# Kernel tuning notes

Hardware: AMD Instinct MI355X
Metric: run time of the kernel (lower is better)

The kernel has to match this reference:

```python
import jax, jax.numpy as jnp
import numpy as np

NEG_INF = -jnp.inf


def _mlp(x, W1, b1, W2, b2, W3, b3):
    h = jax.nn.relu(x @ W1 + b1)
    h = jax.nn.relu(h @ W2 + b2)
    return h @ W3 + b3


def setup_inputs() -> dict:
    key = jax.random.key(0)
    ks = jax.random.split(key, 8)
    B, D, H, A = 65536, 1024, 128, 47
    obs_tensor = jax.random.normal(ks[0], (B, D), jnp.float32)
    action_mask = jax.random.randint(ks[1], (B, 2, A), 0, 2).astype(jnp.int32)
    action_mask = action_mask.at[:, :, 0].set(1)  # pass action always legal
    def lin(k, fan_in, shape):
        s = 1.0 / np.sqrt(fan_in)
        return jax.random.uniform(k, shape, jnp.float32, -s, s)
    W1 = lin(ks[2], D, (D, H)); b1 = lin(ks[3], D, (H,))
    W2 = lin(ks[4], H, (H, H)); b2 = lin(ks[5], H, (H,))
    W3 = lin(ks[6], H, (H, 2 * A)); b3 = lin(ks[7], H, (2 * A,))
    return {"obs_tensor": obs_tensor, "action_mask": action_mask,
            "W1": W1, "b1": b1, "W2": W2, "b2": b2, "W3": W3, "b3": b3}


def reference(obs_tensor, action_mask, W1, b1, W2, b2, W3, b3):
    B = obs_tensor.shape[0]
    A = W3.shape[1] // 2
    logits = _mlp(obs_tensor.reshape(B, -1), W1, b1, W2, b2, W3, b3).reshape(B, 2, A)
    logits = jnp.where(action_mask == 0, NEG_INF, logits)

    fp1 = (action_mask[:, 0].sum(axis=1) == 1) & (action_mask[:, 0, 0] == 1)
    fp2 = (action_mask[:, 1].sum(axis=1) == 1) & (action_mask[:, 1, 0] == 1)

    idx = jnp.arange(A)
    k1, k2 = jax.random.split(jax.random.key(42))
    g1 = jax.random.gumbel(k1, (B, A), jnp.float32)
    g2 = jax.random.gumbel(k2, (B, A), jnp.float32)

    # side 1: when force_pass_2 (and not force_pass_1), index 0 is removed before sampling
    l1 = logits[:, 0]
    l1 = jnp.where((fp2 & ~fp1)[:, None] & (idx[None, :] == 0), NEG_INF, l1)
    a1_sampled = jnp.argmax(l1 + g1, axis=1)
    a1 = jnp.where(fp1, 0, a1_sampled)

    # side 2 extra masking driven by sampled action1 (default branch only)
    switch1 = (a1 >= 1) & (a1 <= 6)
    move1 = (a1 >= 27) & (a1 <= 46)
    extra = (switch1[:, None] & (idx[None, :] == a1[:, None])) | \
            (move1[:, None] & (idx[None, :] >= 27) & (idx[None, :] < 46))
    mask2 = ((fp1 & ~fp2)[:, None] & (idx[None, :] == 0)) | \
            ((~fp1 & ~fp2)[:, None] & extra)
    l2 = jnp.where(mask2, NEG_INF, logits[:, 1])
    a2_sampled = jnp.argmax(l2 + g2, axis=1)
    a2 = jnp.where(fp2, 0, a2_sampled)

    return jnp.stack([a1, a2], axis=1).astype(jnp.int64)
```

## Files before the change

kernel.cpp:

```cpp
#include <hip/hip_runtime.h>

typedef unsigned int u32;
typedef unsigned long long u64;
typedef _Float16 f16;
typedef f16 half8 __attribute__((ext_vector_type(8)));
typedef float f32x4 __attribute__((ext_vector_type(4)));

struct U2 { u32 x, y; };

__host__ __device__ constexpr u32 rotl32(u32 v, int r) {
  return (v << r) | (v >> (32 - r));
}

__host__ __device__ constexpr U2 threefry2x32(u32 k0, u32 k1, u32 c0, u32 c1) {
  u32 ks2 = k0 ^ k1 ^ 0x1BD11BDAu;
  u32 x0 = c0 + k0, x1 = c1 + k1;
#define TFR(r) { x0 += x1; x1 = rotl32(x1, r); x1 ^= x0; }
  TFR(13) TFR(15) TFR(26) TFR(6)
  x0 += k1; x1 += ks2 + 1u;
  TFR(17) TFR(29) TFR(16) TFR(24)
  x0 += ks2; x1 += k0 + 2u;
  TFR(13) TFR(15) TFR(26) TFR(6)
  x0 += k0; x1 += k1 + 3u;
  TFR(17) TFR(29) TFR(16) TFR(24)
  x0 += k1; x1 += ks2 + 4u;
  TFR(13) TFR(15) TFR(26) TFR(6)
  x0 += ks2; x1 += k0 + 5u;
#undef TFR
  return {x0, x1};
}

constexpr U2 SK1 = threefry2x32(0u, 42u, 0u, 0u);
constexpr U2 SK2 = threefry2x32(0u, 42u, 0u, 1u);
constexpr u32 K1A = SK1.x, K1B = SK1.y;
constexpr u32 K2A = SK2.x, K2B = SK2.y;

#define NACT 47

__device__ __forceinline__ float gumbel_at(u32 kA, u32 kB, u32 i) {
  U2 r = threefry2x32(kA, kB, 0u, i);
  u32 bits = r.x ^ r.y;
  float f = __uint_as_float(0x3f800000u | (bits >> 9)) - 1.0f;
  f = fmaxf(f, 1.17549435e-38f);
  return -logf(-logf(f));
}

__device__ __forceinline__ u32 fmono(float f) {
  u32 b = __float_as_uint(f);
  return b ^ ((b & 0x80000000u) ? 0xFFFFFFFFu : 0x80000000u);
}

#define W1H_OFF 0u
#define W1L_OFF 262144u
#define W2H_OFF 524288u
#define W2L_OFF 557056u
#define W3H_OFF 589824u
#define W3L_OFF 614400u
#define WS_NEEDED 638976u

__global__ __launch_bounds__(256)
void prep_weights(const float* __restrict__ W1, const float* __restrict__ W2,
                  const float* __restrict__ W3, char* __restrict__ ws) {
  const int bid = blockIdx.x, t = threadIdx.x;
  if (bid < 512) {
    int idx = bid * 256 + t;
    int col = idx & 127, k = idx >> 7;
    float w = W1[(size_t)k * 128 + col] * 32.0f;
    f16 h = (f16)w;
    f16 l = (f16)((w - (float)h) * 2048.0f);
    u32 addr = (u32)(k >> 6) * 16384u + (u32)(col >> 4) * 2048u +
               (u32)((k >> 5) & 1) * 1024u + (u32)((k >> 3) & 3) * 256u +
               (u32)(col & 15) * 16u + (u32)(k & 7) * 2u;
    *(f16*)(ws + W1H_OFF + addr) = h;
    *(f16*)(ws + W1L_OFF + addr) = l;
  } else if (bid < 576) {
    int idx = (bid - 512) * 256 + t;
    int col = idx & 127, k = idx >> 7;
    float w = W2[(size_t)k * 128 + col] * 32.0f;
    f16 h = (f16)w;
    f16 l = (f16)((w - (float)h) * 2048.0f);
    u32 addr = (u32)(k >> 5) * 8192u + (u32)(col >> 4) * 1024u +
               (u32)((k >> 3) & 3) * 256u + (u32)(col & 15) * 16u + (u32)(k & 7) * 2u;
    *(f16*)(ws + W2H_OFF + addr) = h;
    *(f16*)(ws + W2L_OFF + addr) = l;
  } else {
    int idx = (bid - 576) * 256 + t;
    int col = idx % 96, k = idx / 96;
    float w = (col < 94) ? W3[(size_t)k * 94 + col] * 32.0f : 0.0f;
    f16 h = (f16)w;
    f16 l = (f16)((w - (float)h) * 2048.0f);
    u32 addr = (u32)(k >> 5) * 6144u + (u32)(col >> 4) * 1024u +
               (u32)((k >> 3) & 3) * 256u + (u32)(col & 15) * 16u + (u32)(k & 7) * 2u;
    *(f16*)(ws + W3H_OFF + addr) = h;
    *(f16*)(ws + W3L_OFF + addr) = l;
  }
}

__device__ __forceinline__ f32x4 mfma16(half8 a, half8 b, f32x4 c) {
  return __builtin_amdgcn_mfma_f32_16x16x32_f16(a, b, c, 0, 0, 0);
}

__device__ __forceinline__ void split8(float4 v0, float4 v1, half8& hi, half8& lo) {
  float xs[8] = {v0.x, v0.y, v0.z, v0.w, v1.x, v1.y, v1.z, v1.w};
#pragma unroll
  for (int i = 0; i < 8; i++) {
    f16 h = (f16)xs[i];
    hi[i] = h;
    lo[i] = (f16)((xs[i] - (float)h) * 2048.0f);
  }
}

__device__ __forceinline__ u32 hb_addr(int row, int g8) {
  return (u32)row * 128u + (u32)((g8 ^ (row & 15)) << 3);
}

__global__ __launch_bounds__(256, 4)
void fused_mfma(const float* __restrict__ X, const int* __restrict__ AM,
                const float* __restrict__ b1, const float* __restrict__ b2,
                const float* __restrict__ b3, const char* __restrict__ ws,
                int* __restrict__ out) {
  __shared__ __align__(16) char smem[32768];
  const int t = threadIdx.x;
  const int lane = t & 63, wid = t >> 6;
  const int lrow = lane & 15, g = lane >> 4;
  const int wr = wid & 1, wc = wid >> 1;
  const int rowBase = blockIdx.x * 64;
  float* Hb = (float*)smem;

  f32x4 mainA[2][4], crossA[2][4];
#pragma unroll
  for (int ti = 0; ti < 2; ti++)
#pragma unroll
    for (int tc = 0; tc < 4; tc++)
#pragma unroll
      for (int r = 0; r < 4; r++) { mainA[ti][tc][r] = 0.0f; crossA[ti][tc][r] = 0.0f; }

  {
    const int rowS = t >> 2, gq = t & 3;
    const float* xsrc = X + (size_t)(rowBase + rowS) * 1024 + gq * 8;
    const u32 wadr = (u32)rowS * 72u + (u32)gq * 16u;
    const u32 radr0 = (u32)(32 * wr + lrow) * 72u + (u32)g * 16u;
    const u32 radr1 = (u32)(32 * wr + 16 + lrow) * 72u + (u32)g * 16u;
    const char* wbase = ws + W1H_OFF + (u32)(4 * wc) * 2048u + (u32)g * 256u + (u32)lrow * 16u;

    float4 sx0, sx1;
    sx0 = *(const float4*)(xsrc);
    sx1 = *(const float4*)(xsrc + 4);
    {
      half8 h, l;
      split8(sx0, sx1, h, l);
      *(half8*)(smem + wadr) = h;
      *(half8*)(smem + wadr + 4608) = l;
    }
    sx0 = *(const float4*)(xsrc + 32);
    sx1 = *(const float4*)(xsrc + 36);
    __syncthreads();

    for (int ks = 0; ks < 32; ks++) {
      const u32 cur = (u32)(ks & 1) * 9216u;
      if (ks < 31) {
        const u32 nxt = (u32)((ks + 1) & 1) * 9216u;
        half8 h, l;
        split8(sx0, sx1, h, l);
        *(half8*)(smem + nxt + wadr) = h;
        *(half8*)(smem + nxt + wadr + 4608) = l;
        if (ks < 30) {
          sx0 = *(const float4*)(xsrc + (ks + 2) * 32);
          sx1 = *(const float4*)(xsrc + (ks + 2) * 32 + 4);
        }
      }
      half8 ah0 = *(const half8*)(smem + cur + radr0);
      half8 al0 = *(const half8*)(smem + cur + radr0 + 4608);
      half8 ah1 = *(const half8*)(smem + cur + radr1);
      half8 al1 = *(const half8*)(smem + cur + radr1 + 4608);
      const char* wb = wbase + (u32)(ks >> 1) * 16384u + (u32)(ks & 1) * 1024u;
#pragma unroll
      for (int tc = 0; tc < 4; tc++) {
        half8 bh = *(const half8*)(wb + tc * 2048);
        half8 bl = *(const half8*)(wb + 262144 + tc * 2048);
        mainA[0][tc]  = mfma16(ah0, bh, mainA[0][tc]);
        crossA[0][tc] = mfma16(ah0, bl, crossA[0][tc]);
        crossA[0][tc] = mfma16(al0, bh, crossA[0][tc]);
        mainA[1][tc]  = mfma16(ah1, bh, mainA[1][tc]);
        crossA[1][tc] = mfma16(ah1, bl, crossA[1][tc]);
        crossA[1][tc] = mfma16(al1, bh, crossA[1][tc]);
      }
      __syncthreads();
    }
  }
#pragma unroll
  for (int ti = 0; ti < 2; ti++)
#pragma unroll
    for (int tc = 0; tc < 4; tc++) {
      const int col = 64 * wc + 16 * tc + lrow;
      const int g8 = col >> 3, c7 = col & 7;
      const float bb = b1[col];
#pragma unroll
      for (int r = 0; r < 4; r++) {
        const int row = 32 * wr + 16 * ti + 4 * g + r;
        Hb[hb_addr(row, g8) + c7] =
            fmaxf((mainA[ti][tc][r] + crossA[ti][tc][r] * 4.8828125e-4f) * 0.03125f + bb,
                  0.0f);
        mainA[ti][tc][r] = 0.0f; crossA[ti][tc][r] = 0.0f;
      }
    }
  __syncthreads();

  {
    const char* wbase = ws + W2H_OFF + (u32)(4 * wc) * 1024u + (u32)g * 256u + (u32)lrow * 16u;
    for (int cc = 0; cc < 4; cc++) {
      half8 ah[2], al[2];
#pragma unroll
      for (int ti = 0; ti < 2; ti++) {
        const int row = 32 * wr + 16 * ti + lrow;
        const float* hp = Hb + hb_addr(row, 4 * cc + g);
        split8(*(const float4*)hp, *(const float4*)(hp + 4), ah[ti], al[ti]);
      }
      const char* wb = wbase + (u32)cc * 8192u;
#pragma unroll
      for (int tc = 0; tc < 4; tc++) {
        half8 bh = *(const half8*)(wb + tc * 1024);
        half8 bl = *(const half8*)(wb + 32768 + tc * 1024);
#pragma unroll
        for (int ti = 0; ti < 2; ti++) {
          mainA[ti][tc]  = mfma16(ah[ti], bh, mainA[ti][tc]);
          crossA[ti][tc] = mfma16(ah[ti], bl, crossA[ti][tc]);
          crossA[ti][tc] = mfma16(al[ti], bh, crossA[ti][tc]);
        }
      }
    }
  }
  __syncthreads();
#pragma unroll
  for (int ti = 0; ti < 2; ti++)
#pragma unroll
    for (int tc = 0; tc < 4; tc++) {
      const int col = 64 * wc + 16 * tc + lrow;
      const int g8 = col >> 3, c7 = col & 7;
      const float bb = b2[col];
#pragma unroll
      for (int r = 0; r < 4; r++) {
        const int row = 32 * wr + 16 * ti + 4 * g + r;
        Hb[hb_addr(row, g8) + c7] =
            fmaxf((mainA[ti][tc][r] + crossA[ti][tc][r] * 4.8828125e-4f) * 0.03125f + bb,
                  0.0f);
        mainA[ti][tc][r] = 0.0f; crossA[ti][tc][r] = 0.0f;
      }
    }
  __syncthreads();

  f32x4 main3[2][3], cross3[2][3];
#pragma unroll
  for (int ti = 0; ti < 2; ti++)
#pragma unroll
    for (int tc = 0; tc < 3; tc++)
#pragma unroll
      for (int r = 0; r < 4; r++) { main3[ti][tc][r] = 0.0f; cross3[ti][tc][r] = 0.0f; }
  {
    const char* wbase = ws + W3H_OFF + (u32)(3 * wc) * 1024u + (u32)g * 256u + (u32)lrow * 16u;
    for (int cc = 0; cc < 4; cc++) {
      half8 ah[2], al[2];
#pragma unroll
      for (int ti = 0; ti < 2; ti++) {
        const int row = 32 * wr + 16 * ti + lrow;
        const float* hp = Hb + hb_addr(row, 4 * cc + g);
        split8(*(const float4*)hp, *(const float4*)(hp + 4), ah[ti], al[ti]);
      }
      const char* wb = wbase + (u32)cc * 6144u;
#pragma unroll
      for (int tc = 0; tc < 3; tc++) {
        half8 bh = *(const half8*)(wb + tc * 1024);
        half8 bl = *(const half8*)(wb + 24576 + tc * 1024);
#pragma unroll
        for (int ti = 0; ti < 2; ti++) {
          main3[ti][tc]  = mfma16(ah[ti], bh, main3[ti][tc]);
          cross3[ti][tc] = mfma16(ah[ti], bl, cross3[ti][tc]);
          cross3[ti][tc] = mfma16(al[ti], bh, cross3[ti][tc]);
        }
      }
    }
  }
  __syncthreads();

  float* Ls = (float*)smem;
#pragma unroll
  for (int ti = 0; ti < 2; ti++)
#pragma unroll
    for (int tc = 0; tc < 3; tc++) {
      const int col = 48 * wc + 16 * tc + lrow;
      const float bb = (col < 94) ? b3[col] : 0.0f;
#pragma unroll
      for (int r = 0; r < 4; r++) {
        const int row = 32 * wr + 16 * ti + 4 * g + r;
        Ls[row * 97 + col] =
            (main3[ti][tc][r] + cross3[ti][tc][r] * 4.8828125e-4f) * 0.03125f + bb;
      }
    }
  __syncthreads();

  {
    const int row = 16 * wid + lrow;
    const int q = g;
    const int* amg = AM + (size_t)(rowBase + row) * 94;
    const float* ls = Ls + row * 97;
    const float NI = -__builtin_huge_valf();

    int amv1[12], amv2[12];
    int s0 = 0, s1 = 0;
#pragma unroll
    for (int k = 0; k < 12; k++) {
      const int a = q + 4 * k;
      amv1[k] = (a < NACT) ? amg[a] : 0;
      amv2[k] = (a < NACT) ? amg[NACT + a] : 0;
      s0 += amv1[k]; s1 += amv2[k];
    }
    s0 += __shfl_xor(s0, 16); s0 += __shfl_xor(s0, 32);
    s1 += __shfl_xor(s1, 16); s1 += __shfl_xor(s1, 32);
    const int am0 = amg[0], amN = amg[NACT];
    const bool fp1 = (s0 == 1) && (am0 == 1);
    const bool fp2 = (s1 == 1) && (amN == 1);
    const u32 growA = (u32)(rowBase + row) * 47u;

    u64 best = 0;
#pragma unroll
    for (int k = 0; k < 12; k++) {
      const int a = q + 4 * k;
      if (a >= NACT) break;
      float l = (amv1[k] != 0) ? ls[a] : NI;
      if (fp2 && !fp1 && a == 0) l = NI;
      float v = l + gumbel_at(K1A, K1B, growA + (u32)a);
      u64 key = ((u64)fmono(v) << 6) | (u32)(63 - a);
      if (key > best) best = key;
    }
    u64 o = __shfl_xor(best, 16); if (o > best) best = o;
    o = __shfl_xor(best, 32); if (o > best) best = o;
    const int a1 = fp1 ? 0 : (63 - (int)(best & 63u));

    const bool sw1 = (a1 >= 1) && (a1 <= 6);
    const bool mv1 = (a1 >= 27);
    best = 0;
#pragma unroll
    for (int k = 0; k < 12; k++) {
      const int a = q + 4 * k;
      if (a >= NACT) break;
      float l = (amv2[k] != 0) ? ls[NACT + a] : NI;
      bool extra = (sw1 && a == a1) || (mv1 && a >= 27 && a < 46);
      if ((fp1 && !fp2 && a == 0) || (!fp1 && !fp2 && extra)) l = NI;
      float v = l + gumbel_at(K2A, K2B, growA + (u32)a);
      u64 key = ((u64)fmono(v) << 6) | (u32)(63 - a);
      if (key > best) best = key;
    }
    o = __shfl_xor(best, 16); if (o > best) best = o;
    o = __shfl_xor(best, 32); if (o > best) best = o;
    const int a2 = fp2 ? 0 : (63 - (int)(best & 63u));

    if (q == 0) {
      out[(size_t)(rowBase + row) * 2 + 0] = a1;
      out[(size_t)(rowBase + row) * 2 + 1] = a2;
    }
  }
}

__global__ __launch_bounds__(256)
void fused_policy_v1(const float* __restrict__ X,  const int* __restrict__ AM,
                     const float* __restrict__ W1, const float* __restrict__ b1,
                     const float* __restrict__ W2, const float* __restrict__ b2,
                     const float* __restrict__ W3, const float* __restrict__ b3,
                     int* __restrict__ out) {
  __shared__ alignas(16) char smem[59904];
  float (*HT)[68]   = reinterpret_cast<float (*)[68]>(smem);
  float (*Wst)[128] = reinterpret_cast<float (*)[128]>(smem + 34816);
  float (*Ws3)[96]  = reinterpret_cast<float (*)[96]>(smem + 34816);
  float (*Xt)[68]   = reinterpret_cast<float (*)[68]>(smem + 51200);
  float (*Lsr)[97]  = reinterpret_cast<float (*)[97]>(smem);
  int*   Amf        = reinterpret_cast<int*>(smem + 34816);

  const int t = threadIdx.x;
  const int rowBase = blockIdx.x * 64;
  const int tx = t & 31, ty = t >> 5;
  const int c0 = tx * 4, r0 = ty * 8;

  float accf[8][4]; double accd[8][4];
#pragma unroll
  for (int i = 0; i < 8; i++)
#pragma unroll
    for (int j = 0; j < 4; j++) { accf[i][j] = 0.0f; accd[i][j] = 0.0; }

  for (int k0 = 0; k0 < 1024; k0 += 32) {
#pragma unroll
    for (int i = 0; i < 2; i++) {
      int idx = t + i * 256;
      int row = idx >> 3, kb = (idx & 7) * 4;
      float4 v = *reinterpret_cast<const float4*>(X + (size_t)(rowBase + row) * 1024 + k0 + kb);
      Xt[kb + 0][row] = v.x; Xt[kb + 1][row] = v.y;
      Xt[kb + 2][row] = v.z; Xt[kb + 3][row] = v.w;
    }
#pragma unroll
    for (int i = 0; i < 4; i++) {
      int idx = t + i * 256;
      int kr = idx >> 5, c4 = (idx & 31) * 4;
      *reinterpret_cast<float4*>(&Wst[kr][c4]) =
          *reinterpret_cast<const float4*>(W1 + (size_t)(k0 + kr) * 128 + c4);
    }
    __syncthreads();
#pragma unroll
    for (int kk = 0; kk < 32; kk++) {
      float4 a0 = *reinterpret_cast<const float4*>(&Xt[kk][r0]);
      float4 a1 = *reinterpret_cast<const float4*>(&Xt[kk][r0 + 4]);
      float4 b  = *reinterpret_cast<const float4*>(&Wst[kk][c0]);
      float av[8] = {a0.x, a0.y, a0.z, a0.w, a1.x, a1.y, a1.z, a1.w};
      float bv[4] = {b.x, b.y, b.z, b.w};
#pragma unroll
      for (int i = 0; i < 8; i++)
#pragma unroll
        for (int j = 0; j < 4; j++) accf[i][j] = fmaf(av[i], bv[j], accf[i][j]);
    }
    if ((k0 & 63) == 32) {
#pragma unroll
      for (int i = 0; i < 8; i++)
#pragma unroll
        for (int j = 0; j < 4; j++) { accd[i][j] += (double)accf[i][j]; accf[i][j] = 0.0f; }
    }
    __syncthreads();
  }
  {
    const float4 bv = *reinterpret_cast<const float4*>(b1 + c0);
#pragma unroll
    for (int i = 0; i < 8; i++) {
      HT[c0 + 0][r0 + i] = fmaxf((float)accd[i][0] + bv.x, 0.0f);
      HT[c0 + 1][r0 + i] = fmaxf((float)accd[i][1] + bv.y, 0.0f);
      HT[c0 + 2][r0 + i] = fmaxf((float)accd[i][2] + bv.z, 0.0f);
      HT[c0 + 3][r0 + i] = fmaxf((float)accd[i][3] + bv.w, 0.0f);
    }
  }
  __syncthreads();

#pragma unroll
  for (int i = 0; i < 8; i++)
#pragma unroll
    for (int j = 0; j < 4; j++) { accf[i][j] = 0.0f; accd[i][j] = 0.0; }
  for (int k0 = 0; k0 < 128; k0 += 32) {
#pragma unroll
    for (int i = 0; i < 4; i++) {
      int idx = t + i * 256;
      int kr = idx >> 5, c4 = (idx & 31) * 4;
      *reinterpret_cast<float4*>(&Wst[kr][c4]) =
          *reinterpret_cast<const float4*>(W2 + (size_t)(k0 + kr) * 128 + c4);
    }
    __syncthreads();
#pragma unroll
    for (int kk = 0; kk < 32; kk++) {
      float4 a0 = *reinterpret_cast<const float4*>(&HT[k0 + kk][r0]);
      float4 a1 = *reinterpret_cast<const float4*>(&HT[k0 + kk][r0 + 4]);
      float4 b  = *reinterpret_cast<const float4*>(&Wst[kk][c0]);
      float av[8] = {a0.x, a0.y, a0.z, a0.w, a1.x, a1.y, a1.z, a1.w};
      float bv[4] = {b.x, b.y, b.z, b.w};
#pragma unroll
      for (int i = 0; i < 8; i++)
#pragma unroll
        for (int j = 0; j < 4; j++) accf[i][j] = fmaf(av[i], bv[j], accf[i][j]);
    }
    if ((k0 & 63) == 32) {
#pragma unroll
      for (int i = 0; i < 8; i++)
#pragma unroll
        for (int j = 0; j < 4; j++) { accd[i][j] += (double)accf[i][j]; accf[i][j] = 0.0f; }
    }
    __syncthreads();
  }
  {
    const float4 bv = *reinterpret_cast<const float4*>(b2 + c0);
#pragma unroll
    for (int i = 0; i < 8; i++) {
      HT[c0 + 0][r0 + i] = fmaxf((float)accd[i][0] + bv.x, 0.0f);
      HT[c0 + 1][r0 + i] = fmaxf((float)accd[i][1] + bv.y, 0.0f);
      HT[c0 + 2][r0 + i] = fmaxf((float)accd[i][2] + bv.z, 0.0f);
      HT[c0 + 3][r0 + i] = fmaxf((float)accd[i][3] + bv.w, 0.0f);
    }
  }
  __syncthreads();

  const int c3 = tx * 3;
  float acc3f[8][3]; double acc3d[8][3];
#pragma unroll
  for (int i = 0; i < 8; i++)
#pragma unroll
    for (int j = 0; j < 3; j++) { acc3f[i][j] = 0.0f; acc3d[i][j] = 0.0; }
  for (int k0 = 0; k0 < 128; k0 += 32) {
#pragma unroll
    for (int i = 0; i < 12; i++) {
      int idx = t + i * 256;
      int kr = idx / 96, c = idx - kr * 96;
      Ws3[kr][c] = (c < 94) ? W3[(size_t)(k0 + kr) * 94 + c] : 0.0f;
    }
    __syncthreads();
#pragma unroll
    for (int kk = 0; kk < 32; kk++) {
      float4 a0 = *reinterpret_cast<const float4*>(&HT[k0 + kk][r0]);
      float4 a1 = *reinterpret_cast<const float4*>(&HT[k0 + kk][r0 + 4]);
      float b0 = Ws3[kk][c3], b1v = Ws3[kk][c3 + 1], b2v = Ws3[kk][c3 + 2];
      float av[8] = {a0.x, a0.y, a0.z, a0.w, a1.x, a1.y, a1.z, a1.w};
      float bv3[3] = {b0, b1v, b2v};
#pragma unroll
      for (int i = 0; i < 8; i++)
#pragma unroll
        for (int j = 0; j < 3; j++) acc3f[i][j] = fmaf(av[i], bv3[j], acc3f[i][j]);
    }
    if ((k0 & 63) == 32) {
#pragma unroll
      for (int i = 0; i < 8; i++)
#pragma unroll
        for (int j = 0; j < 3; j++) { acc3d[i][j] += (double)acc3f[i][j]; acc3f[i][j] = 0.0f; }
    }
    __syncthreads();
  }
  {
    float b3v[3];
#pragma unroll
    for (int j = 0; j < 3; j++) b3v[j] = (c3 + j < 94) ? b3[c3 + j] : 0.0f;
#pragma unroll
    for (int i = 0; i < 8; i++)
#pragma unroll
      for (int j = 0; j < 3; j++)
        Lsr[r0 + i][c3 + j] = (float)acc3d[i][j] + b3v[j];
  }
#pragma unroll
  for (int i = 0; i < 24; i++) {
    int idx = t + i * 256;
    if (idx < 64 * 94) Amf[idx] = AM[(size_t)rowBase * 94 + idx];
  }
  __syncthreads();

  if (t < 64) {
    const int row = rowBase + t;
    const float NI = -__builtin_huge_valf();
    const int* am = Amf + t * 94;
    int sum0 = 0, sum1 = 0;
    for (int a = 0; a < NACT; a++) { sum0 += am[a]; sum1 += am[NACT + a]; }
    const bool fp1 = (sum0 == 1) && (am[0] == 1);
    const bool fp2 = (sum1 == 1) && (am[NACT] == 1);
    float bestv = NI; int a1s = 0;
    for (int a = 0; a < NACT; a++) {
      float l = (am[a] != 0) ? Lsr[t][a] : NI;
      if (fp2 && !fp1 && a == 0) l = NI;
      float v = l + gumbel_at(K1A, K1B, (u32)row * 47u + (u32)a);
      if (v > bestv) { bestv = v; a1s = a; }
    }
    const int a1 = fp1 ? 0 : a1s;
    const bool sw1 = (a1 >= 1) && (a1 <= 6);
    const bool mv1 = (a1 >= 27) && (a1 <= 46);
    bestv = NI; int a2s = 0;
    for (int a = 0; a < NACT; a++) {
      float l = (am[NACT + a] != 0) ? Lsr[t][NACT + a] : NI;
      bool extra = (sw1 && a == a1) || (mv1 && a >= 27 && a < 46);
      bool m2 = (fp1 && !fp2 && a == 0) || (!fp1 && !fp2 && extra);
      if (m2) l = NI;
      float v = l + gumbel_at(K2A, K2B, (u32)row * 47u + (u32)a);
      if (v > bestv) { bestv = v; a2s = a; }
    }
    const int a2 = fp2 ? 0 : a2s;
    out[(size_t)row * 2 + 0] = a1;
    out[(size_t)row * 2 + 1] = a2;
  }
}

extern "C" void kernel_launch(void* const* d_in, const int* in_sizes, int n_in,
                              void* d_out, int out_size, void* d_ws, size_t ws_size,
                              hipStream_t stream) {
  const float* X  = (const float*)d_in[0];
  const int*   AM = (const int*)d_in[1];
  const float* W1 = (const float*)d_in[2];
  const float* b1 = (const float*)d_in[3];
  const float* W2 = (const float*)d_in[4];
  const float* b2 = (const float*)d_in[5];
  const float* W3 = (const float*)d_in[6];
  const float* b3 = (const float*)d_in[7];
  int* out = (int*)d_out;

  if (ws_size >= (size_t)WS_NEEDED) {
    prep_weights<<<624, 256, 0, stream>>>(W1, W2, W3, (char*)d_ws);
    fused_mfma<<<1024, 256, 0, stream>>>(X, AM, b1, b2, b3, (const char*)d_ws, out);
  } else {
    fused_policy_v1<<<1024, 256, 0, stream>>>(X, AM, W1, b1, W2, b2, W3, b3, out);
  }
}
```

Before: 133.4 us.

## Halve rows per block to 32 and split columns across four waves

Shrinks the row tile of the fused MLP kernel from 64 to 32 rows per block and launches twice as many blocks. Each wave now covers 32 output columns for all 32 rows instead of a 2x2 row/column split, and shared memory is halved. The sampling epilogue is remapped to 8 lanes per row. The aim is more blocks per CU and better occupancy and latency hiding, at the cost of each block re-reading the W1 weights for half as many rows, which roughly doubles weight traffic per unit of work.

```diff
diff --git a/kernel.cpp b/kernel.cpp
--- a/kernel.cpp
+++ b/kernel.cpp
@@ -4,6 +4,7 @@
 typedef unsigned long long u64;
 typedef _Float16 f16;
 typedef f16 half8 __attribute__((ext_vector_type(8)));
+typedef f16 half4 __attribute__((ext_vector_type(4)));
 typedef float f32x4 __attribute__((ext_vector_type(4)));
 
 struct U2 { u32 x, y; };
@@ -110,6 +111,16 @@
   }
 }
 
+__device__ __forceinline__ void split4(float4 v, half4& hi, half4& lo) {
+  float xs[4] = {v.x, v.y, v.z, v.w};
+#pragma unroll
+  for (int i = 0; i < 4; i++) {
+    f16 h = (f16)xs[i];
+    hi[i] = h;
+    lo[i] = (f16)((xs[i] - (float)h) * 2048.0f);
+  }
+}
+
 __device__ __forceinline__ u32 hb_addr(int row, int g8) {
   return (u32)row * 128u + (u32)((g8 ^ (row & 15)) << 3);
 }
@@ -119,63 +130,58 @@
                 const float* __restrict__ b1, const float* __restrict__ b2,
                 const float* __restrict__ b3, const char* __restrict__ ws,
                 int* __restrict__ out) {
-  __shared__ __align__(16) char smem[32768];
+  __shared__ __align__(16) char smem[16384];
   const int t = threadIdx.x;
   const int lane = t & 63, wid = t >> 6;
   const int lrow = lane & 15, g = lane >> 4;
-  const int wr = wid & 1, wc = wid >> 1;
-  const int rowBase = blockIdx.x * 64;
+  const int wc = wid;
+  const int rowBase = blockIdx.x * 32;
   float* Hb = (float*)smem;
 
-  f32x4 mainA[2][4], crossA[2][4];
+  f32x4 mainA[2][2], crossA[2][2];
 #pragma unroll
   for (int ti = 0; ti < 2; ti++)
 #pragma unroll
-    for (int tc = 0; tc < 4; tc++)
+    for (int tc = 0; tc < 2; tc++)
 #pragma unroll
       for (int r = 0; r < 4; r++) { mainA[ti][tc][r] = 0.0f; crossA[ti][tc][r] = 0.0f; }
 
   {
-    const int rowS = t >> 2, gq = t & 3;
-    const float* xsrc = X + (size_t)(rowBase + rowS) * 1024 + gq * 8;
-    const u32 wadr = (u32)rowS * 72u + (u32)gq * 16u;
-    const u32 radr0 = (u32)(32 * wr + lrow) * 72u + (u32)g * 16u;
-    const u32 radr1 = (u32)(32 * wr + 16 + lrow) * 72u + (u32)g * 16u;
-    const char* wbase = ws + W1H_OFF + (u32)(4 * wc) * 2048u + (u32)g * 256u + (u32)lrow * 16u;
-
-    float4 sx0, sx1;
-    sx0 = *(const float4*)(xsrc);
-    sx1 = *(const float4*)(xsrc + 4);
+    const int rowS = t >> 3, q = t & 7;
+    const float* xsrc = X + (size_t)(rowBase + rowS) * 1024 + q * 4;
+    const u32 wadr = (u32)rowS * 72u + (u32)q * 8u;
+    const u32 radr0 = (u32)lrow * 72u + (u32)g * 16u;
+    const u32 radr1 = (u32)(16 + lrow) * 72u + (u32)g * 16u;
+    const char* wbase = ws + W1H_OFF + (u32)(2 * wc) * 2048u + (u32)g * 256u + (u32)lrow * 16u;
+
+    float4 sx;
+    sx = *(const float4*)(xsrc);
     {
-      half8 h, l;
-      split8(sx0, sx1, h, l);
-      *(half8*)(smem + wadr) = h;
-      *(half8*)(smem + wadr + 4608) = l;
-    }
-    sx0 = *(const float4*)(xsrc + 32);
-    sx1 = *(const float4*)(xsrc + 36);
+      half4 h, l;
+      split4(sx, h, l);
+      *(half4*)(smem + wadr) = h;
+      *(half4*)(smem + wadr + 2304) = l;
+    }
+    sx = *(const float4*)(xsrc + 32);
     __syncthreads();
 
     for (int ks = 0; ks < 32; ks++) {
-      const u32 cur = (u32)(ks & 1) * 9216u;
+      const u32 cur = (u32)(ks & 1) * 4608u;
       if (ks < 31) {
-        const u32 nxt = (u32)((ks + 1) & 1) * 9216u;
-        half8 h, l;
-        split8(sx0, sx1, h, l);
-        *(half8*)(smem + nxt + wadr) = h;
-        *(half8*)(smem + nxt + wadr + 4608) = l;
-        if (ks < 30) {
-          sx0 = *(const float4*)(xsrc + (ks + 2) * 32);
-          sx1 = *(const float4*)(xsrc + (ks + 2) * 32 + 4);
-        }
+        const u32 nxt = (u32)((ks + 1) & 1) * 4608u;
+        half4 h, l;
+        split4(sx, h, l);
+        *(half4*)(smem + nxt + wadr) = h;
+        *(half4*)(smem + nxt + wadr + 2304) = l;
+        if (ks < 30) sx = *(const float4*)(xsrc + (ks + 2) * 32);
       }
       half8 ah0 = *(const half8*)(smem + cur + radr0);
-      half8 al0 = *(const half8*)(smem + cur + radr0 + 4608);
+      half8 al0 = *(const half8*)(smem + cur + radr0 + 2304);
       half8 ah1 = *(const half8*)(smem + cur + radr1);
-      half8 al1 = *(const half8*)(smem + cur + radr1 + 4608);
+      half8 al1 = *(const half8*)(smem + cur + radr1 + 2304);
       const char* wb = wbase + (u32)(ks >> 1) * 16384u + (u32)(ks & 1) * 1024u;
 #pragma unroll
-      for (int tc = 0; tc < 4; tc++) {
+      for (int tc = 0; tc < 2; tc++) {
         half8 bh = *(const half8*)(wb + tc * 2048);
         half8 bl = *(const half8*)(wb + 262144 + tc * 2048);
         mainA[0][tc]  = mfma16(ah0, bh, mainA[0][tc]);
@@ -191,13 +197,13 @@
 #pragma unroll
   for (int ti = 0; ti < 2; ti++)
 #pragma unroll
-    for (int tc = 0; tc < 4; tc++) {
-      const int col = 64 * wc + 16 * tc + lrow;
+    for (int tc = 0; tc < 2; tc++) {
+      const int col = 32 * wc + 16 * tc + lrow;
       const int g8 = col >> 3, c7 = col & 7;
       const float bb = b1[col];
 #pragma unroll
       for (int r = 0; r < 4; r++) {
-        const int row = 32 * wr + 16 * ti + 4 * g + r;
+        const int row = 16 * ti + 4 * g + r;
         Hb[hb_addr(row, g8) + c7] =
             fmaxf((mainA[ti][tc][r] + crossA[ti][tc][r] * 4.8828125e-4f) * 0.03125f + bb,
                   0.0f);
@@ -207,18 +213,18 @@
   __syncthreads();
 
   {
-    const char* wbase = ws + W2H_OFF + (u32)(4 * wc) * 1024u + (u32)g * 256u + (u32)lrow * 16u;
+    const char* wbase = ws + W2H_OFF + (u32)(2 * wc) * 1024u + (u32)g * 256u + (u32)lrow * 16u;
     for (int cc = 0; cc < 4; cc++) {
       half8 ah[2], al[2];
 #pragma unroll
       for (int ti = 0; ti < 2; ti++) {
-        const int row = 32 * wr + 16 * ti + lrow;
+        const int row = 16 * ti + lrow;
         const float* hp = Hb + hb_addr(row, 4 * cc + g);
         split8(*(const float4*)hp, *(const float4*)(hp + 4), ah[ti], al[ti]);
       }
       const char* wb = wbase + (u32)cc * 8192u;
 #pragma unroll
-      for (int tc = 0; tc < 4; tc++) {
+      for (int tc = 0; tc < 2; tc++) {
         half8 bh = *(const half8*)(wb + tc * 1024);
         half8 bl = *(const half8*)(wb + 32768 + tc * 1024);
 #pragma unroll
@@ -234,13 +240,13 @@
 #pragma unroll
   for (int ti = 0; ti < 2; ti++)
 #pragma unroll
-    for (int tc = 0; tc < 4; tc++) {
-      const int col = 64 * wc + 16 * tc + lrow;
+    for (int tc = 0; tc < 2; tc++) {
+      const int col = 32 * wc + 16 * tc + lrow;
       const int g8 = col >> 3, c7 = col & 7;
       const float bb = b2[col];
 #pragma unroll
       for (int r = 0; r < 4; r++) {
-        const int row = 32 * wr + 16 * ti + 4 * g + r;
+        const int row = 16 * ti + 4 * g + r;
         Hb[hb_addr(row, g8) + c7] =
             fmaxf((mainA[ti][tc][r] + crossA[ti][tc][r] * 4.8828125e-4f) * 0.03125f + bb,
                   0.0f);
@@ -249,33 +255,36 @@
     }
   __syncthreads();
 
-  f32x4 main3[2][3], cross3[2][3];
+  f32x4 main3[2][2], cross3[2][2];
 #pragma unroll
   for (int ti = 0; ti < 2; ti++)
 #pragma unroll
-    for (int tc = 0; tc < 3; tc++)
+    for (int tc = 0; tc < 2; tc++)
 #pragma unroll
       for (int r = 0; r < 4; r++) { main3[ti][tc][r] = 0.0f; cross3[ti][tc][r] = 0.0f; }
   {
-    const char* wbase = ws + W3H_OFF + (u32)(3 * wc) * 1024u + (u32)g * 256u + (u32)lrow * 16u;
     for (int cc = 0; cc < 4; cc++) {
       half8 ah[2], al[2];
 #pragma unroll
       for (int ti = 0; ti < 2; ti++) {
-        const int row = 32 * wr + 16 * ti + lrow;
+        const int row = 16 * ti + lrow;
         const float* hp = Hb + hb_addr(row, 4 * cc + g);
         split8(*(const float4*)hp, *(const float4*)(hp + 4), ah[ti], al[ti]);
       }
-      const char* wb = wbase + (u32)cc * 6144u;
-#pragma unroll
-      for (int tc = 0; tc < 3; tc++) {
-        half8 bh = *(const half8*)(wb + tc * 1024);
-        half8 bl = *(const half8*)(wb + 24576 + tc * 1024);
-#pragma unroll
-        for (int ti = 0; ti < 2; ti++) {
-          main3[ti][tc]  = mfma16(ah[ti], bh, main3[ti][tc]);
-          cross3[ti][tc] = mfma16(ah[ti], bl, cross3[ti][tc]);
-          cross3[ti][tc] = mfma16(al[ti], bh, cross3[ti][tc]);
+#pragma unroll
+      for (int tc = 0; tc < 2; tc++) {
+        const int tt = 2 * wc + tc;
+        if (tt < 6) {
+          const char* wb = ws + W3H_OFF + (u32)cc * 6144u + (u32)tt * 1024u +
+                           (u32)g * 256u + (u32)lrow * 16u;
+          half8 bh = *(const half8*)(wb);
+          half8 bl = *(const half8*)(wb + 24576);
+#pragma unroll
+          for (int ti = 0; ti < 2; ti++) {
+            main3[ti][tc]  = mfma16(ah[ti], bh, main3[ti][tc]);
+            cross3[ti][tc] = mfma16(ah[ti], bl, cross3[ti][tc]);
+            cross3[ti][tc] = mfma16(al[ti], bh, cross3[ti][tc]);
+          }
         }
       }
     }
@@ -286,36 +295,39 @@
 #pragma unroll
   for (int ti = 0; ti < 2; ti++)
 #pragma unroll
-    for (int tc = 0; tc < 3; tc++) {
-      const int col = 48 * wc + 16 * tc + lrow;
-      const float bb = (col < 94) ? b3[col] : 0.0f;
-#pragma unroll
-      for (int r = 0; r < 4; r++) {
-        const int row = 32 * wr + 16 * ti + 4 * g + r;
-        Ls[row * 97 + col] =
-            (main3[ti][tc][r] + cross3[ti][tc][r] * 4.8828125e-4f) * 0.03125f + bb;
+    for (int tc = 0; tc < 2; tc++) {
+      const int tt = 2 * wc + tc;
+      if (tt < 6) {
+        const int col = 16 * tt + lrow;
+        const float bb = (col < 94) ? b3[col] : 0.0f;
+#pragma unroll
+        for (int r = 0; r < 4; r++) {
+          const int row = 16 * ti + 4 * g + r;
+          Ls[row * 97 + col] =
+              (main3[ti][tc][r] + cross3[ti][tc][r] * 4.8828125e-4f) * 0.03125f + bb;
+        }
       }
     }
   __syncthreads();
 
   {
-    const int row = 16 * wid + lrow;
-    const int q = g;
+    const int row = (wid << 3) + (lane >> 3);
+    const int q = lane & 7;
     const int* amg = AM + (size_t)(rowBase + row) * 94;
     const float* ls = Ls + row * 97;
     const float NI = -__builtin_huge_valf();
 
-    int amv1[12], amv2[12];
+    int amv1[6], amv2[6];
     int s0 = 0, s1 = 0;
 #pragma unroll
-    for (int k = 0; k < 12; k++) {
-      const int a = q + 4 * k;
+    for (int k = 0; k < 6; k++) {
+      const int a = q + 8 * k;
       amv1[k] = (a < NACT) ? amg[a] : 0;
       amv2[k] = (a < NACT) ? amg[NACT + a] : 0;
       s0 += amv1[k]; s1 += amv2[k];
     }
-    s0 += __shfl_xor(s0, 16); s0 += __shfl_xor(s0, 32);
-    s1 += __shfl_xor(s1, 16); s1 += __shfl_xor(s1, 32);
+    s0 += __shfl_xor(s0, 1); s0 += __shfl_xor(s0, 2); s0 += __shfl_xor(s0, 4);
+    s1 += __shfl_xor(s1, 1); s1 += __shfl_xor(s1, 2); s1 += __shfl_xor(s1, 4);
     const int am0 = amg[0], amN = amg[NACT];
     const bool fp1 = (s0 == 1) && (am0 == 1);
     const bool fp2 = (s1 == 1) && (amN == 1);
@@ -323,8 +335,8 @@
 
     u64 best = 0;
 #pragma unroll
-    for (int k = 0; k < 12; k++) {
-      const int a = q + 4 * k;
+    for (int k = 0; k < 6; k++) {
+      const int a = q + 8 * k;
       if (a >= NACT) break;
       float l = (amv1[k] != 0) ? ls[a] : NI;
       if (fp2 && !fp1 && a == 0) l = NI;
@@ -332,16 +344,17 @@
       u64 key = ((u64)fmono(v) << 6) | (u32)(63 - a);
       if (key > best) best = key;
     }
-    u64 o = __shfl_xor(best, 16); if (o > best) best = o;
-    o = __shfl_xor(best, 32); if (o > best) best = o;
+    u64 o = __shfl_xor(best, 1); if (o > best) best = o;
+    o = __shfl_xor(best, 2); if (o > best) best = o;
+    o = __shfl_xor(best, 4); if (o > best) best = o;
     const int a1 = fp1 ? 0 : (63 - (int)(best & 63u));
 
     const bool sw1 = (a1 >= 1) && (a1 <= 6);
     const bool mv1 = (a1 >= 27);
     best = 0;
 #pragma unroll
-    for (int k = 0; k < 12; k++) {
-      const int a = q + 4 * k;
+    for (int k = 0; k < 6; k++) {
+      const int a = q + 8 * k;
       if (a >= NACT) break;
       float l = (amv2[k] != 0) ? ls[NACT + a] : NI;
       bool extra = (sw1 && a == a1) || (mv1 && a >= 27 && a < 46);
@@ -350,8 +363,9 @@
       u64 key = ((u64)fmono(v) << 6) | (u32)(63 - a);
       if (key > best) best = key;
     }
-    o = __shfl_xor(best, 16); if (o > best) best = o;
-    o = __shfl_xor(best, 32); if (o > best) best = o;
+    o = __shfl_xor(best, 1); if (o > best) best = o;
+    o = __shfl_xor(best, 2); if (o > best) best = o;
+    o = __shfl_xor(best, 4); if (o > best) best = o;
     const int a2 = fp2 ? 0 : (63 - (int)(best & 63u));
 
     if (q == 0) {
@@ -579,7 +593,7 @@
 
   if (ws_size >= (size_t)WS_NEEDED) {
     prep_weights<<<624, 256, 0, stream>>>(W1, W2, W3, (char*)d_ws);
-    fused_mfma<<<1024, 256, 0, stream>>>(X, AM, b1, b2, b3, (const char*)d_ws, out);
+    fused_mfma<<<2048, 256, 0, stream>>>(X, AM, b1, b2, b3, (const char*)d_ws, out);
   } else {
     fused_policy_v1<<<1024, 256, 0, stream>>>(X, AM, W1, b1, W2, b2, W3, b3, out);
   }
```

After: 130.3 us. 2.3% less time.
